# Performance work log

Hardware: AMD Instinct MI355X
Metric: run time of the kernel (lower is better)

Reference implementation:

```python
import jax, jax.numpy as jnp
import numpy as np

L = 8          # number of QTT cores = log2(init_reso)
RESO = 256     # init_reso
MAX_RANK = 256
N_SAMPLES = 4096


def _qtt_ranks(L, max_rank):
    return [min(8 ** k, 8 ** (L - k), max_rank) for k in range(L + 1)]


def setup_inputs() -> dict:
    key = jax.random.key(0)
    ranks = _qtt_ranks(L, MAX_RANK)
    keys = jax.random.split(key, L + 1)
    inp = {}
    for l in range(L):
        shape = (ranks[l], 8, ranks[l + 1])
        scale = (shape[0] * shape[1]) ** -0.5  # keep chain products O(1)
        inp[f"core{l}"] = jax.random.normal(keys[l], shape, dtype=jnp.float32) * scale
    inp["coords_xyz"] = jax.random.randint(keys[L], (N_SAMPLES, 3), 0, RESO)
    return inp


def _coords_to_qtt(coords_xyz, num_cores):
    # coords_xyz: (N, 3) int. Per core l (most-significant bit first):
    # c_l = 4*bit_x + 2*bit_y + bit_z in [0, 8)  -> shape (L, N)
    x, y, z = coords_xyz[:, 0], coords_xyz[:, 1], coords_xyz[:, 2]
    shifts = jnp.arange(num_cores - 1, -1, -1)[:, None]  # (L, 1)
    bx = (x[None, :] >> shifts) & 1
    by = (y[None, :] >> shifts) & 1
    bz = (z[None, :] >> shifts) & 1
    return 4 * bx + 2 * by + bz


def _sample_tt(cores, coords):
    # cores[l]: (r_l, 8, r_{l+1}); coords: (L, N)
    # v starts as first core slice: (N, r_1)  (r_0 == 1)
    v = cores[0][0, coords[0], :]
    for l in range(1, len(cores)):
        # gathered slice: (r_l, N, r_{l+1}) -> (N, r_l, r_{l+1})
        g = jnp.transpose(cores[l][:, coords[l], :], (1, 0, 2))
        v = jnp.einsum('nr,nrs->ns', v, g)
    return v[:, 0]  # r_L == 1 -> (N,)


def reference(core0, core1, core2, core3, core4, core5, core6, core7, coords_xyz):
    cores = [core0, core1, core2, core3, core4, core5, core6, core7]
    coords = _coords_to_qtt(coords_xyz, len(cores))
    return _sample_tt(cores, coords)
```

## Files before the change

### kernel.cpp

```cpp
#include <hip/hip_runtime.h>


typedef unsigned int u32;

__device__ __forceinline__ void async_load16(const float* g, float* l) {
    __builtin_amdgcn_global_load_lds(
        (const __attribute__((address_space(1))) u32*)g,
        (__attribute__((address_space(3))) u32*)l, 16, 0, 0);
}
__device__ __forceinline__ void fma4(float4& c, float a, const float4& b) {
    c.x = fmaf(a, b.x, c.x); c.y = fmaf(a, b.y, c.y);
    c.z = fmaf(a, b.z, c.z); c.w = fmaf(a, b.w, c.w);
}
__device__ __forceinline__ int digit_of(int x, int y, int z, int sh) {
    return 4*((x>>sh)&1) + 2*((y>>sh)&1) + ((z>>sh)&1);
}

__global__ __launch_bounds__(256, 4) void tables_kernel(
    const float* __restrict__ C0, const float* __restrict__ C1,
    const float* __restrict__ C2, const float* __restrict__ C3,
    const float* __restrict__ C5, const float* __restrict__ C6,
    const float* __restrict__ C7,
    const int* __restrict__ coords, int n,
    int* __restrict__ perms, int* __restrict__ bases,
    float* __restrict__ P3, float* __restrict__ T)
{
    __shared__ __align__(16) union {
        struct { unsigned char digs[8192]; int cnt[8]; int offs[8]; } p;
        struct { float S6s[8][64]; } b;
        struct { float v64[8][64]; float As[8][260]; float Bs[2][16][256]; } g;
    } u;
    const int t = threadIdx.x;
    const int ln = t & 63, wv = t >> 6;
    const int bx = blockIdx.x;

    if (bx == 0) {
        if (t < 8) u.p.cnt[t] = 0;
        __syncthreads();
        for (int i = t; i < n; i += 256) {
            const int d = digit_of(coords[3*i], coords[3*i+1], coords[3*i+2], 3);
            u.p.digs[i] = (unsigned char)d;
            atomicAdd(&u.p.cnt[d], 1);
        }
        __syncthreads();
        if (t == 0) {
            int run = 0;
            for (int d = 0; d < 8; ++d) {
                u.p.offs[d] = run;
                bases[d] = run;
                run += u.p.cnt[d];
            }
            bases[8] = run;
        }
        __syncthreads();
        for (int i = t; i < n; i += 256) {
            const int pos = atomicAdd(&u.p.offs[u.p.digs[i]], 1);
            perms[pos] = i;
        }
    } else if (bx < 65) {
        const int bb = bx - 1;
        const int d5 = bb >> 3, d6 = bb & 7;
#pragma unroll
        for (int j = 0; j < 2; ++j) {
            const int idx = t + 256*j, d7 = idx >> 6, s = idx & 63;
            float acc = 0.f;
#pragma unroll
            for (int jj = 0; jj < 8; ++jj)
                acc = fmaf(C6[s*64 + d6*8 + jj], C7[jj*8 + d7], acc);
            u.b.S6s[d7][s] = acc;
        }
        __syncthreads();
        float4 creg[16];
#pragma unroll
        for (int s4 = 0; s4 < 16; ++s4)
            creg[s4] = *(const float4*)(C5 + (size_t)t*512 + d5*64 + s4*4);
#pragma unroll 1
        for (int d7 = 0; d7 < 8; ++d7) {
            float acc = 0.f;
#pragma unroll
            for (int s4 = 0; s4 < 16; ++s4) {
                const float4 a = creg[s4];
                const float4 b = *(const float4*)&u.b.S6s[d7][s4*4];
                acc = fmaf(a.x, b.x, acc); acc = fmaf(a.y, b.y, acc);
                acc = fmaf(a.z, b.z, acc); acc = fmaf(a.w, b.w, acc);
            }
            T[(size_t)((d5*8 + d6)*8 + d7)*256 + t] = acc;
        }
    } else {
        const int bb = bx - 65;
        const int d3 = bb & 7, d2 = (bb >> 3) & 7, d0 = bb >> 6;
        const float* Cd = C3 + d3 * 256;

        for (int r = wv; r < 16; r += 4)
            async_load16(Cd + (size_t)r*2048 + ln*4, &u.g.Bs[0][r][ln*4]);

#pragma unroll
        for (int j = 0; j < 2; ++j) {
            const int idx = t + 256*j, d1 = idx >> 6, c = idx & 63;
            float acc = 0.f;
#pragma unroll
            for (int r = 0; r < 8; ++r)
                acc = fmaf(C0[d0*8 + r], C1[r*512 + d1*64 + c], acc);
            u.g.v64[d1][c] = acc;
        }
        __syncthreads();

        {
            float4 accA0 = make_float4(0,0,0,0), accA1 = make_float4(0,0,0,0);
#pragma unroll 8
            for (int j = 0; j < 64; ++j) {
                const float4 c2 = *(const float4*)(C2 + (size_t)j*2048 + d2*256 + ln*4);
                fma4(accA0, u.g.v64[wv*2 + 0][j], c2);
                fma4(accA1, u.g.v64[wv*2 + 1][j], c2);
            }
            *(float4*)&u.g.As[wv*2 + 0][ln*4] = accA0;
            *(float4*)&u.g.As[wv*2 + 1][ln*4] = accA1;
        }
        __syncthreads();

        float4 acc0 = make_float4(0,0,0,0), acc1 = make_float4(0,0,0,0);
        for (int c = 0; c < 16; ++c) {
            if (c + 1 < 16) {
                const int nb = (c+1) & 1;
                for (int r = wv; r < 16; r += 4)
                    async_load16(Cd + (size_t)((c+1)*16 + r)*2048 + ln*4,
                                 &u.g.Bs[nb][r][ln*4]);
            }
            const int cb = c & 1, kb = c * 16;
#pragma unroll 1
            for (int k4 = 0; k4 < 16; k4 += 4) {
                const float4 a0 = *(const float4*)&u.g.As[wv*2 + 0][kb + k4];
                const float4 a1 = *(const float4*)&u.g.As[wv*2 + 1][kb + k4];
                const float4 b0v = *(const float4*)&u.g.Bs[cb][k4+0][ln*4];
                const float4 b1v = *(const float4*)&u.g.Bs[cb][k4+1][ln*4];
                const float4 b2v = *(const float4*)&u.g.Bs[cb][k4+2][ln*4];
                const float4 b3v = *(const float4*)&u.g.Bs[cb][k4+3][ln*4];
                fma4(acc0, a0.x, b0v); fma4(acc0, a0.y, b1v);
                fma4(acc0, a0.z, b2v); fma4(acc0, a0.w, b3v);
                fma4(acc1, a1.x, b0v); fma4(acc1, a1.y, b1v);
                fma4(acc1, a1.z, b2v); fma4(acc1, a1.w, b3v);
            }
            __syncthreads();
        }
        {
            const int a0i = d0*512 + (wv*2 + 0)*64 + d2*8 + d3;
            const int a1i = d0*512 + (wv*2 + 1)*64 + d2*8 + d3;
            *(float4*)(P3 + (size_t)a0i*256 + ln*4) = acc0;
            *(float4*)(P3 + (size_t)a1i*256 + ln*4) = acc1;
        }
    }
}

__global__ __launch_bounds__(256, 4) void stage4_final_kernel(
    const float* __restrict__ P3, const float* __restrict__ C4,
    const float* __restrict__ T, const int* __restrict__ coords,
    const int* __restrict__ perm, const int* __restrict__ base,
    float* __restrict__ out)
{
    const int d = blockIdx.x;
    const int b0 = base[d], b1 = base[d + 1];
    const int nrows = b1 - b0;
    const int t = threadIdx.x, ln = t & 63, wv = t >> 6;

    __shared__ __align__(16) float Arm[8][260];
    __shared__ __align__(16) float Bs[2][16][256];
    __shared__ int rows[8], aidx[8], qs[8];

    const float* Cd = C4 + d * 256;

    for (int tile = blockIdx.y; tile * 8 < nrows; tile += (int)gridDim.y) {
        const int row0 = b0 + tile * 8;

        for (int r = wv; r < 16; r += 4)
            async_load16(Cd + (size_t)r*2048 + ln*4, &Bs[0][r][ln*4]);
        if (t < 8) {
            const int gr = row0 + t;
            const int rr = (gr < b1) ? perm[gr] : -1;
            rows[t] = rr;
            int a = 0, q = 0;
            if (rr >= 0) {
                const int x = coords[3*rr], y = coords[3*rr+1], z = coords[3*rr+2];
                a = digit_of(x,y,z,7)*512 + digit_of(x,y,z,6)*64
                  + digit_of(x,y,z,5)*8 + digit_of(x,y,z,4);
                q = digit_of(x,y,z,2)*64 + digit_of(x,y,z,1)*8 + digit_of(x,y,z,0);
            }
            aidx[t] = a; qs[t] = q;
        }
        __syncthreads();

#pragma unroll
        for (int j = 0; j < 2; ++j) {
            const int idx = t + 256*j, s = idx >> 6, c4 = idx & 63;
            float4 v = make_float4(0,0,0,0);
            if (rows[s] >= 0)
                v = *(const float4*)(P3 + (size_t)aidx[s]*256 + c4*4);
            *(float4*)&Arm[s][c4*4] = v;
        }
        __syncthreads();

        float4 acc0 = make_float4(0,0,0,0), acc1 = make_float4(0,0,0,0);

        for (int c = 0; c < 16; ++c) {
            if (c + 1 < 16) {
                const int nb = (c+1) & 1;
                for (int r = wv; r < 16; r += 4)
                    async_load16(Cd + (size_t)((c+1)*16 + r)*2048 + ln*4,
                                 &Bs[nb][r][ln*4]);
            }
            const int cb = c & 1, kb = c * 16;
#pragma unroll 1
            for (int k4 = 0; k4 < 16; k4 += 4) {
                const float4 a0 = *(const float4*)&Arm[wv*2 + 0][kb + k4];
                const float4 a1 = *(const float4*)&Arm[wv*2 + 1][kb + k4];
                const float4 b0v = *(const float4*)&Bs[cb][k4+0][ln*4];
                const float4 b1v = *(const float4*)&Bs[cb][k4+1][ln*4];
                const float4 b2v = *(const float4*)&Bs[cb][k4+2][ln*4];
                const float4 b3v = *(const float4*)&Bs[cb][k4+3][ln*4];
                fma4(acc0, a0.x, b0v); fma4(acc0, a0.y, b1v);
                fma4(acc0, a0.z, b2v); fma4(acc0, a0.w, b3v);
                fma4(acc1, a1.x, b0v); fma4(acc1, a1.y, b1v);
                fma4(acc1, a1.z, b2v); fma4(acc1, a1.w, b3v);
            }
            __syncthreads();
        }

#pragma unroll
        for (int i = 0; i < 2; ++i) {
            const int s = wv*2 + i;
            const int rr = rows[s];
            float p = 0.f;
            if (rr >= 0) {
                const float4 a = (i == 0) ? acc0 : acc1;
                const float4 tv = *(const float4*)(T + (size_t)qs[s]*256 + ln*4);
                p = fmaf(a.x, tv.x, fmaf(a.y, tv.y, fmaf(a.z, tv.z, a.w * tv.w)));
            }
            p += __shfl_xor(p, 1);
            p += __shfl_xor(p, 2);
            p += __shfl_xor(p, 4);
            p += __shfl_xor(p, 8);
            p += __shfl_xor(p, 16);
            p += __shfl_xor(p, 32);
            if (ln == 0 && rr >= 0) out[rr] = p;
        }
        __syncthreads();
    }
}

extern "C" void kernel_launch(void* const* d_in, const int* in_sizes, int n_in,
                              void* d_out, int out_size, void* d_ws, size_t ws_size,
                              hipStream_t stream) {
    const float* C0 = (const float*)d_in[0];
    const float* C1 = (const float*)d_in[1];
    const float* C2 = (const float*)d_in[2];
    const float* C3 = (const float*)d_in[3];
    const float* C4 = (const float*)d_in[4];
    const float* C5 = (const float*)d_in[5];
    const float* C6 = (const float*)d_in[6];
    const float* C7 = (const float*)d_in[7];
    const int* coords = (const int*)d_in[8];
    float* out = (float*)d_out;

    const int n = in_sizes[8] / 3;

    float* P3   = (float*)d_ws;
    float* Tt   = P3 + 4096*256;
    int*   perms = (int*)(Tt + 512*256);
    int*   bases = perms + (size_t)n;

    tables_kernel<<<577, 256, 0, stream>>>(
        C0, C1, C2, C3, C5, C6, C7, coords, n, perms, bases, P3, Tt);
    stage4_final_kernel<<<dim3(8, 64), 256, 0, stream>>>(
        P3, C4, Tt, coords, perms, bases, out);
}
```

Measured before the change: 125.4 us.

## Fuse table and stage-4 kernels into one persistent kernel with grid barrier

Merges the two launches into a single 512-block kernel. Each block first builds its share of the tables (T, P3), and the 8-way bucket sort of sample indices is now split across 8 blocks instead of running on one. A global atomic spin barrier then separates that phase from the stage-4 contraction. This removes the second launch and the gap between kernels and spreads the sort work. In exchange, correctness depends on all 512 blocks being resident at once. The barrier counter is only reset when the workspace holds the poison value 0xAAAAAAAA, so repeated calls on an unpoisoned workspace would fall through the barrier and race.

```diff
diff --git a/kernel.cpp b/kernel.cpp
--- a/kernel.cpp
+++ b/kernel.cpp
@@ -2,6 +2,9 @@
 
 
 typedef unsigned int u32;
+
+#define NBLK 512u
+#define POISON 0xAAAAAAAAu
 
 __device__ __forceinline__ void async_load16(const float* g, float* l) {
     __builtin_amdgcn_global_load_lds(
@@ -16,50 +19,30 @@
     return 4*((x>>sh)&1) + 2*((y>>sh)&1) + ((z>>sh)&1);
 }
 
-__global__ __launch_bounds__(256, 4) void tables_kernel(
+__global__ __launch_bounds__(256, 4) void fused_kernel(
     const float* __restrict__ C0, const float* __restrict__ C1,
     const float* __restrict__ C2, const float* __restrict__ C3,
-    const float* __restrict__ C5, const float* __restrict__ C6,
-    const float* __restrict__ C7,
+    const float* __restrict__ C4, const float* __restrict__ C5,
+    const float* __restrict__ C6, const float* __restrict__ C7,
     const int* __restrict__ coords, int n,
     int* __restrict__ perms, int* __restrict__ bases,
-    float* __restrict__ P3, float* __restrict__ T)
+    float* __restrict__ P3, float* __restrict__ T,
+    u32* __restrict__ bar, float* __restrict__ out)
 {
     __shared__ __align__(16) union {
-        struct { unsigned char digs[8192]; int cnt[8]; int offs[8]; } p;
+        struct { int cnt[8]; int mybase; int rank; } p;
         struct { float S6s[8][64]; } b;
         struct { float v64[8][64]; float As[8][260]; float Bs[2][16][256]; } g;
+        struct { float Arm[8][260]; float Bs[2][16][256]; } s4;
     } u;
+    __shared__ int rows[8], aidx[8], qs[8];
+
     const int t = threadIdx.x;
     const int ln = t & 63, wv = t >> 6;
     const int bx = blockIdx.x;
 
-    if (bx == 0) {
-        if (t < 8) u.p.cnt[t] = 0;
-        __syncthreads();
-        for (int i = t; i < n; i += 256) {
-            const int d = digit_of(coords[3*i], coords[3*i+1], coords[3*i+2], 3);
-            u.p.digs[i] = (unsigned char)d;
-            atomicAdd(&u.p.cnt[d], 1);
-        }
-        __syncthreads();
-        if (t == 0) {
-            int run = 0;
-            for (int d = 0; d < 8; ++d) {
-                u.p.offs[d] = run;
-                bases[d] = run;
-                run += u.p.cnt[d];
-            }
-            bases[8] = run;
-        }
-        __syncthreads();
-        for (int i = t; i < n; i += 256) {
-            const int pos = atomicAdd(&u.p.offs[u.p.digs[i]], 1);
-            perms[pos] = i;
-        }
-    } else if (bx < 65) {
-        const int bb = bx - 1;
-        const int d5 = bb >> 3, d6 = bb & 7;
+    if (bx < 64) {
+        const int d5 = bx >> 3, d6 = bx & 7;
 #pragma unroll
         for (int j = 0; j < 2; ++j) {
             const int idx = t + 256*j, d7 = idx >> 6, s = idx & 63;
@@ -72,23 +55,25 @@
         __syncthreads();
         float4 creg[16];
 #pragma unroll
-        for (int s4 = 0; s4 < 16; ++s4)
-            creg[s4] = *(const float4*)(C5 + (size_t)t*512 + d5*64 + s4*4);
+        for (int s4i = 0; s4i < 16; ++s4i)
+            creg[s4i] = *(const float4*)(C5 + (size_t)t*512 + d5*64 + s4i*4);
 #pragma unroll 1
         for (int d7 = 0; d7 < 8; ++d7) {
             float acc = 0.f;
 #pragma unroll
-            for (int s4 = 0; s4 < 16; ++s4) {
-                const float4 a = creg[s4];
-                const float4 b = *(const float4*)&u.b.S6s[d7][s4*4];
+            for (int s4i = 0; s4i < 16; ++s4i) {
+                const float4 a = creg[s4i];
+                const float4 b = *(const float4*)&u.b.S6s[d7][s4i*4];
                 acc = fmaf(a.x, b.x, acc); acc = fmaf(a.y, b.y, acc);
                 acc = fmaf(a.z, b.z, acc); acc = fmaf(a.w, b.w, acc);
             }
             T[(size_t)((d5*8 + d6)*8 + d7)*256 + t] = acc;
         }
-    } else {
-        const int bb = bx - 65;
-        const int d3 = bb & 7, d2 = (bb >> 3) & 7, d0 = bb >> 6;
+        __syncthreads();
+    }
+
+    {
+        const int d3 = bx & 7, d2 = (bx >> 3) & 7, d0 = bx >> 6;
         const float* Cd = C3 + d3 * 256;
 
         for (int r = wv; r < 16; r += 4)
@@ -106,15 +91,15 @@
         __syncthreads();
 
         {
-            float4 accA0 = make_float4(0,0,0,0), accA1 = make_float4(0,0,0,0);
+            float4 a0 = make_float4(0,0,0,0), a1 = make_float4(0,0,0,0);
 #pragma unroll 8
             for (int j = 0; j < 64; ++j) {
                 const float4 c2 = *(const float4*)(C2 + (size_t)j*2048 + d2*256 + ln*4);
-                fma4(accA0, u.g.v64[wv*2 + 0][j], c2);
-                fma4(accA1, u.g.v64[wv*2 + 1][j], c2);
-            }
-            *(float4*)&u.g.As[wv*2 + 0][ln*4] = accA0;
-            *(float4*)&u.g.As[wv*2 + 1][ln*4] = accA1;
+                fma4(a0, u.g.v64[wv*2 + 0][j], c2);
+                fma4(a1, u.g.v64[wv*2 + 1][j], c2);
+            }
+            *(float4*)&u.g.As[wv*2 + 0][ln*4] = a0;
+            *(float4*)&u.g.As[wv*2 + 1][ln*4] = a1;
         }
         __syncthreads();
 
@@ -149,100 +134,136 @@
             *(float4*)(P3 + (size_t)a1i*256 + ln*4) = acc1;
         }
     }
-}
-
-__global__ __launch_bounds__(256, 4) void stage4_final_kernel(
-    const float* __restrict__ P3, const float* __restrict__ C4,
-    const float* __restrict__ T, const int* __restrict__ coords,
-    const int* __restrict__ perm, const int* __restrict__ base,
-    float* __restrict__ out)
-{
-    const int d = blockIdx.x;
-    const int b0 = base[d], b1 = base[d + 1];
-    const int nrows = b1 - b0;
-    const int t = threadIdx.x, ln = t & 63, wv = t >> 6;
-
-    __shared__ __align__(16) float Arm[8][260];
-    __shared__ __align__(16) float Bs[2][16][256];
-    __shared__ int rows[8], aidx[8], qs[8];
-
-    const float* Cd = C4 + d * 256;
-
-    for (int tile = blockIdx.y; tile * 8 < nrows; tile += (int)gridDim.y) {
-        const int row0 = b0 + tile * 8;
-
-        for (int r = wv; r < 16; r += 4)
-            async_load16(Cd + (size_t)r*2048 + ln*4, &Bs[0][r][ln*4]);
-        if (t < 8) {
-            const int gr = row0 + t;
-            const int rr = (gr < b1) ? perm[gr] : -1;
-            rows[t] = rr;
-            int a = 0, q = 0;
-            if (rr >= 0) {
-                const int x = coords[3*rr], y = coords[3*rr+1], z = coords[3*rr+2];
-                a = digit_of(x,y,z,7)*512 + digit_of(x,y,z,6)*64
-                  + digit_of(x,y,z,5)*8 + digit_of(x,y,z,4);
-                q = digit_of(x,y,z,2)*64 + digit_of(x,y,z,1)*8 + digit_of(x,y,z,0);
-            }
-            aidx[t] = a; qs[t] = q;
-        }
-        __syncthreads();
-
-#pragma unroll
-        for (int j = 0; j < 2; ++j) {
-            const int idx = t + 256*j, s = idx >> 6, c4 = idx & 63;
-            float4 v = make_float4(0,0,0,0);
-            if (rows[s] >= 0)
-                v = *(const float4*)(P3 + (size_t)aidx[s]*256 + c4*4);
-            *(float4*)&Arm[s][c4*4] = v;
-        }
-        __syncthreads();
-
-        float4 acc0 = make_float4(0,0,0,0), acc1 = make_float4(0,0,0,0);
-
-        for (int c = 0; c < 16; ++c) {
-            if (c + 1 < 16) {
-                const int nb = (c+1) & 1;
-                for (int r = wv; r < 16; r += 4)
-                    async_load16(Cd + (size_t)((c+1)*16 + r)*2048 + ln*4,
-                                 &Bs[nb][r][ln*4]);
-            }
-            const int cb = c & 1, kb = c * 16;
+
+    if (bx >= 64 && bx < 72) {
+        const int d = bx - 64;
+        __syncthreads();
+        if (t < 8) u.p.cnt[t] = 0;
+        if (t == 8) u.p.rank = 0;
+        __syncthreads();
+        for (int i = t; i < n; i += 256) {
+            const int dg = digit_of(coords[3*i], coords[3*i+1], coords[3*i+2], 3);
+            atomicAdd(&u.p.cnt[dg], 1);
+        }
+        __syncthreads();
+        if (t == 0) {
+            int run = 0;
+            for (int dd = 0; dd < 8; ++dd) {
+                if (dd == d) u.p.mybase = run;
+                if (d == 0) bases[dd] = run;
+                run += u.p.cnt[dd];
+            }
+            if (d == 0) bases[8] = run;
+        }
+        __syncthreads();
+        const int mb = u.p.mybase;
+        for (int i = t; i < n; i += 256) {
+            const int dg = digit_of(coords[3*i], coords[3*i+1], coords[3*i+2], 3);
+            if (dg == d) {
+                const int pos = atomicAdd(&u.p.rank, 1);
+                perms[mb + pos] = i;
+            }
+        }
+    }
+
+    __threadfence();
+    __syncthreads();
+    if (t == 0) {
+        atomicCAS(bar, POISON, 0u);
+        atomicAdd(bar, 1u);
+        u32 spins = 0;
+        while (__hip_atomic_load(bar, __ATOMIC_RELAXED, __HIP_MEMORY_SCOPE_AGENT)
+               < NBLK) {
+            __builtin_amdgcn_s_sleep(16);
+            if (++spins > (1u << 26)) break;
+        }
+    }
+    __syncthreads();
+    __threadfence();
+
+    {
+        const int d  = bx & 7;
+        const int ty = bx >> 3;
+        const int b0 = bases[d], b1 = bases[d + 1];
+        const int nrows = b1 - b0;
+        const float* Cd = C4 + d * 256;
+
+        for (int tile = ty; tile * 8 < nrows; tile += 64) {
+            const int row0 = b0 + tile * 8;
+
+            for (int r = wv; r < 16; r += 4)
+                async_load16(Cd + (size_t)r*2048 + ln*4, &u.s4.Bs[0][r][ln*4]);
+            if (t < 8) {
+                const int gr = row0 + t;
+                const int rr = (gr < b1) ? perms[gr] : -1;
+                rows[t] = rr;
+                int a = 0, q = 0;
+                if (rr >= 0) {
+                    const int x = coords[3*rr], y = coords[3*rr+1], z = coords[3*rr+2];
+                    a = digit_of(x,y,z,7)*512 + digit_of(x,y,z,6)*64
+                      + digit_of(x,y,z,5)*8 + digit_of(x,y,z,4);
+                    q = digit_of(x,y,z,2)*64 + digit_of(x,y,z,1)*8 + digit_of(x,y,z,0);
+                }
+                aidx[t] = a; qs[t] = q;
+            }
+            __syncthreads();
+
+#pragma unroll
+            for (int j = 0; j < 2; ++j) {
+                const int idx = t + 256*j, s = idx >> 6, c4 = idx & 63;
+                float4 v = make_float4(0,0,0,0);
+                if (rows[s] >= 0)
+                    v = *(const float4*)(P3 + (size_t)aidx[s]*256 + c4*4);
+                *(float4*)&u.s4.Arm[s][c4*4] = v;
+            }
+            __syncthreads();
+
+            float4 acc0 = make_float4(0,0,0,0), acc1 = make_float4(0,0,0,0);
+
+            for (int c = 0; c < 16; ++c) {
+                if (c + 1 < 16) {
+                    const int nb = (c+1) & 1;
+                    for (int r = wv; r < 16; r += 4)
+                        async_load16(Cd + (size_t)((c+1)*16 + r)*2048 + ln*4,
+                                     &u.s4.Bs[nb][r][ln*4]);
+                }
+                const int cb = c & 1, kb = c * 16;
 #pragma unroll 1
-            for (int k4 = 0; k4 < 16; k4 += 4) {
-                const float4 a0 = *(const float4*)&Arm[wv*2 + 0][kb + k4];
-                const float4 a1 = *(const float4*)&Arm[wv*2 + 1][kb + k4];
-                const float4 b0v = *(const float4*)&Bs[cb][k4+0][ln*4];
-                const float4 b1v = *(const float4*)&Bs[cb][k4+1][ln*4];
-                const float4 b2v = *(const float4*)&Bs[cb][k4+2][ln*4];
-                const float4 b3v = *(const float4*)&Bs[cb][k4+3][ln*4];
-                fma4(acc0, a0.x, b0v); fma4(acc0, a0.y, b1v);
-                fma4(acc0, a0.z, b2v); fma4(acc0, a0.w, b3v);
-                fma4(acc1, a1.x, b0v); fma4(acc1, a1.y, b1v);
-                fma4(acc1, a1.z, b2v); fma4(acc1, a1.w, b3v);
-            }
-            __syncthreads();
-        }
-
-#pragma unroll
-        for (int i = 0; i < 2; ++i) {
-            const int s = wv*2 + i;
-            const int rr = rows[s];
-            float p = 0.f;
-            if (rr >= 0) {
-                const float4 a = (i == 0) ? acc0 : acc1;
-                const float4 tv = *(const float4*)(T + (size_t)qs[s]*256 + ln*4);
-                p = fmaf(a.x, tv.x, fmaf(a.y, tv.y, fmaf(a.z, tv.z, a.w * tv.w)));
-            }
-            p += __shfl_xor(p, 1);
-            p += __shfl_xor(p, 2);
-            p += __shfl_xor(p, 4);
-            p += __shfl_xor(p, 8);
-            p += __shfl_xor(p, 16);
-            p += __shfl_xor(p, 32);
-            if (ln == 0 && rr >= 0) out[rr] = p;
-        }
-        __syncthreads();
+                for (int k4 = 0; k4 < 16; k4 += 4) {
+                    const float4 a0 = *(const float4*)&u.s4.Arm[wv*2 + 0][kb + k4];
+                    const float4 a1 = *(const float4*)&u.s4.Arm[wv*2 + 1][kb + k4];
+                    const float4 b0v = *(const float4*)&u.s4.Bs[cb][k4+0][ln*4];
+                    const float4 b1v = *(const float4*)&u.s4.Bs[cb][k4+1][ln*4];
+                    const float4 b2v = *(const float4*)&u.s4.Bs[cb][k4+2][ln*4];
+                    const float4 b3v = *(const float4*)&u.s4.Bs[cb][k4+3][ln*4];
+                    fma4(acc0, a0.x, b0v); fma4(acc0, a0.y, b1v);
+                    fma4(acc0, a0.z, b2v); fma4(acc0, a0.w, b3v);
+                    fma4(acc1, a1.x, b0v); fma4(acc1, a1.y, b1v);
+                    fma4(acc1, a1.z, b2v); fma4(acc1, a1.w, b3v);
+                }
+                __syncthreads();
+            }
+
+#pragma unroll
+            for (int i = 0; i < 2; ++i) {
+                const int s = wv*2 + i;
+                const int rr = rows[s];
+                float p = 0.f;
+                if (rr >= 0) {
+                    const float4 a = (i == 0) ? acc0 : acc1;
+                    const float4 tv = *(const float4*)(T + (size_t)qs[s]*256 + ln*4);
+                    p = fmaf(a.x, tv.x, fmaf(a.y, tv.y, fmaf(a.z, tv.z, a.w * tv.w)));
+                }
+                p += __shfl_xor(p, 1);
+                p += __shfl_xor(p, 2);
+                p += __shfl_xor(p, 4);
+                p += __shfl_xor(p, 8);
+                p += __shfl_xor(p, 16);
+                p += __shfl_xor(p, 32);
+                if (ln == 0 && rr >= 0) out[rr] = p;
+            }
+            __syncthreads();
+        }
     }
 }
 
@@ -266,9 +287,9 @@
     float* Tt   = P3 + 4096*256;
     int*   perms = (int*)(Tt + 512*256);
     int*   bases = perms + (size_t)n;
-
-    tables_kernel<<<577, 256, 0, stream>>>(
-        C0, C1, C2, C3, C5, C6, C7, coords, n, perms, bases, P3, Tt);
-    stage4_final_kernel<<<dim3(8, 64), 256, 0, stream>>>(
-        P3, C4, Tt, coords, perms, bases, out);
-}
+    u32*   bar   = (u32*)(bases + 16);
+
+    fused_kernel<<<NBLK, 256, 0, stream>>>(
+        C0, C1, C2, C3, C4, C5, C6, C7, coords, n,
+        perms, bases, P3, Tt, bar, out);
+}
```

After: 234.0 us. 1.87x slower.
